# Performance work log

Hardware: AMD Instinct MI355X
Metric: run time of the kernel (lower is better)

The kernel has to match this reference:

```python
import jax, jax.numpy as jnp
import numpy as np

MUL = 32          # multiplicity of 0e and 1o channels
NRAD = 8          # radial basis size
NPATH = 7         # TP instructions

# Orthonormal symmetric-traceless basis for the real l=2 irrep -> Cartesian map
_B = np.zeros((5, 3, 3))
_s2 = 1.0 / np.sqrt(2.0)
_B[0, 0, 1] = _B[0, 1, 0] = _s2                      # xy
_B[1, 1, 2] = _B[1, 2, 1] = _s2                      # yz
_B[2] = np.diag([-1.0, -1.0, 2.0]) / np.sqrt(6.0)    # 2z^2-x^2-y^2
_B[3, 0, 2] = _B[3, 2, 0] = _s2                      # xz
_B[4] = np.diag([1.0, -1.0, 0.0]) / np.sqrt(2.0)     # x^2-y^2
# w3j(1,2,1)[i,M,k], Frobenius-normalized to 1 (e3nn convention)
C121 = jnp.asarray(np.transpose(_B, (1, 0, 2)) / np.sqrt(5.0), jnp.float32)
INV_SQRT3 = float(1.0 / np.sqrt(3.0))   # w3j(1,1,0) / w3j(0,1,1) / w3j(1,0,1)
A0 = float(1.0 / np.sqrt(64.0))         # path weight, l=0 outs: sqrt(1/fan_in), fan_in=2*32
A1 = float(np.sqrt(3.0 / 96.0))         # path weight, l=1 out: sqrt((2l+1)/fan_in), fan_in=3*32


def setup_inputs() -> dict:
    key = jax.random.key(0)
    ks = jax.random.split(key, 9)
    N, E = 4096, 32768
    x = jax.random.normal(ks[0], (N, 4 * MUL), jnp.float32)
    edge_attr = jax.random.normal(ks[1], (E, 9), jnp.float32)
    edge_length = jax.random.uniform(ks[2], (E,), jnp.float32) * 5.0
    edge_src = jax.random.randint(ks[3], (E,), 0, N)
    edge_dst = jax.random.randint(ks[4], (E,), 0, N)
    W_fc1 = jax.random.normal(ks[5], (NRAD, 64), jnp.float32)
    W_fc2 = jax.random.normal(ks[6], (64, NPATH * MUL * MUL), jnp.float32)
    W_sc_s = jax.random.normal(ks[7], (MUL, MUL), jnp.float32)
    W_sc_v = jax.random.normal(ks[8], (MUL, MUL), jnp.float32)
    return dict(x=x, edge_attr=edge_attr, edge_length=edge_length,
                edge_src=edge_src, edge_dst=edge_dst,
                W_fc1=W_fc1, W_fc2=W_fc2, W_sc_s=W_sc_s, W_sc_v=W_sc_v)


def reference(x, edge_attr, edge_length, edge_src, edge_dst, W_fc1, W_fc2, W_sc_s, W_sc_v):
    N = x.shape[0]
    # radial Gaussian basis: centers linspace(0,5,8), sigma = spacing
    centers = jnp.linspace(0.0, 5.0, NRAD)
    sigma = 5.0 / (NRAD - 1)
    d = edge_length[:, None] - centers[None, :]
    radial = jnp.exp(-d * d / (2.0 * sigma * sigma))
    # radial MLP -> per-edge TP weights (e3nn FullyConnectedNet: W/sqrt(fan_in), silu)
    h = jax.nn.silu(radial @ (W_fc1 / jnp.sqrt(jnp.float32(NRAD))))
    w = h @ (W_fc2 / jnp.sqrt(jnp.float32(64)))          # [E, 7168]
    W = w.reshape(-1, NPATH, MUL, MUL)                    # [E,7,u,w]
    # split node features: 32x0e scalars + 32x1o vectors
    s = x[:, :MUL]
    v = x[:, MUL:].reshape(N, MUL, 3)
    sj = s[edge_src]                                      # [E,u]
    vj = v[edge_src]                                      # [E,u,3]
    y0 = edge_attr[:, 0]
    y1 = edge_attr[:, 1:4]
    y2 = edge_attr[:, 4:9]
    # tensor-product paths
    t00 = sj * y0[:, None]                                            # 0e x 0e
    t11 = jnp.einsum('eui,ei->eu', vj, y1) * INV_SQRT3                # 1o x 1o -> 0e
    out_s = (jnp.einsum('eu,euw->ew', t00, W[:, 0]) +
             jnp.einsum('eu,euw->ew', t11, W[:, 1])) * A0             # scalars
    out_g = (jnp.einsum('eu,euw->ew', t00, W[:, 2]) +
             jnp.einsum('eu,euw->ew', t11, W[:, 3])) * A0             # gates
    t01 = sj[:, :, None] * y1[:, None, :] * INV_SQRT3                 # 0e x 1o -> 1o
    t10 = vj * (y0[:, None, None] * INV_SQRT3)                        # 1o x 0e -> 1o
    t12 = jnp.einsum('eui,imk,em->euk', vj, C121, y2)                 # 1o x 2e -> 1o
    out_v = (jnp.einsum('euk,euw->ewk', t01, W[:, 4]) +
             jnp.einsum('euk,euw->ewk', t10, W[:, 5]) +
             jnp.einsum('euk,euw->ewk', t12, W[:, 6])) * A1           # [E,w,3]
    m_ij = jnp.concatenate([out_s, out_g, out_v.reshape(-1, 3 * MUL)], axis=1)  # [E,160]
    # scatter-mean over destination nodes
    sums = jax.ops.segment_sum(m_ij, edge_dst, num_segments=N)
    cnt = jax.ops.segment_sum(jnp.ones((m_ij.shape[0],), m_ij.dtype), edge_dst, num_segments=N)
    m_i = sums / jnp.clip(cnt, 1.0)[:, None]
    # gate: silu on scalars, sigmoid gates multiply the 1o block per-channel
    gs = jax.nn.silu(m_i[:, :MUL])
    gate = jax.nn.sigmoid(m_i[:, MUL:2 * MUL])
    gv = m_i[:, 2 * MUL:].reshape(N, MUL, 3) * gate[:, :, None]
    # residual self-connection (e3nn o3.Linear: per-irrep, / sqrt(mul_in))
    inv_sqrt_mul = 1.0 / jnp.sqrt(jnp.float32(MUL))
    h_s = gs + (s @ W_sc_s) * inv_sqrt_mul
    h_v = gv + jnp.einsum('nui,uw->nwi', v, W_sc_v) * inv_sqrt_mul
    # o3.Norm: per-irrep L2 norm over the (2l+1) components
    norm_s = jnp.sqrt(h_s * h_s + 1e-12)
    norm_v = jnp.sqrt(jnp.sum(h_v * h_v, axis=-1) + 1e-12)
    return jnp.concatenate([norm_s, norm_v], axis=1)       # [N, 64]
```

## Files before the change

### kernel.cpp

```cpp
#include <hip/hip_runtime.h>

#define NIVL  256
#define KINV  51.2f
#define KSTEP 0.01953125f
#define TPW   7168
#define BCAP  256
#define DCAP  64
#define NROW  11
#define TSTR  40

typedef __attribute__((ext_vector_type(8))) __bf16 bf16x8;
typedef __attribute__((ext_vector_type(4))) float f32x4;
union FragU { uint4 u; bf16x8 v; };

__device__ __forceinline__ float sigmoidf_(float v) { return 1.f / (1.f + expf(-v)); }
__device__ __forceinline__ unsigned bf16r_(float x) { return (__float_as_uint(x) + 0x8000u) >> 16; }
__device__ __forceinline__ unsigned pk_(float lo, float hi) { return (bf16r_(hi) << 16) | bf16r_(lo); }

__device__ __forceinline__ f32x4 mfma_(bf16x8 a, bf16x8 b, f32x4 c) {
    return __builtin_amdgcn_mfma_f32_16x16x32_bf16(a, b, c, 0, 0, 0);
}

__global__ __launch_bounds__(256)
void prep_kernel(const float* __restrict__ W1, const float* __restrict__ W2,
                 const float* __restrict__ elen, const int* __restrict__ edst,
                 float* __restrict__ T, int* __restrict__ cntL, int* __restrict__ cntD,
                 int* __restrict__ sortedL, int* __restrict__ sortedD, int E)
{
    const int tid = threadIdx.x;
    if (blockIdx.x < 231) {
        __shared__ float hk_s[8][64];
        const int bx = blockIdx.x % 7;
        const int k0 = (blockIdx.x / 7) * 8;
        const int pw = bx * 1024 + tid * 4;
#pragma unroll
        for (int q = 0; q < 2; ++q) {
            int idx = tid + q * 256;
            int kk = idx >> 6, c = idx & 63;
            float L = (float)(k0 + kk) * KSTEP;
            float d = 0.f;
#pragma unroll
            for (int r = 0; r < 8; ++r) {
                float dd = L - (float)r * (5.f / 7.f);
                d += expf(-dd * dd * 0.98f) * W1[r * 64 + c];
            }
            d *= 0.3535533906f;
            hk_s[kk][c] = d * sigmoidf_(d) * 0.125f;
        }
        __syncthreads();
        float4 acc[8];
#pragma unroll
        for (int q = 0; q < 8; ++q) acc[q] = make_float4(0.f, 0.f, 0.f, 0.f);
        for (int c = 0; c < 64; ++c) {
            float4 w4 = *(const float4*)(W2 + (size_t)c * TPW + pw);
#pragma unroll
            for (int q = 0; q < 8; ++q) {
                float hv = hk_s[q][c];
                acc[q].x = fmaf(hv, w4.x, acc[q].x);
                acc[q].y = fmaf(hv, w4.y, acc[q].y);
                acc[q].z = fmaf(hv, w4.z, acc[q].z);
                acc[q].w = fmaf(hv, w4.w, acc[q].w);
            }
        }
#pragma unroll
        for (int q = 0; q < 8; ++q) {
            int k = k0 + q;
            if (k < 257)
                *(float4*)(T + (size_t)k * TPW + pw) = acc[q];
        }
    } else {
        int e = (blockIdx.x - 231) * 256 + tid;
        if (e < E) {
            float t = elen[e] * KINV;
            int j = (int)t; j = j > 255 ? 255 : j;
            int pos = atomicAdd(&cntL[j], 1);
            if (pos < BCAP) sortedL[j * BCAP + pos] = e;
            int d = edst[e];
            int pd = atomicAdd(&cntD[d], 1);
            if (pd < DCAP) sortedD[d * DCAP + pd] = e;
        }
    }
}

__global__ __launch_bounds__(256, 2)
void fold_kernel(const float* __restrict__ x, const float* __restrict__ ea,
                 const float* __restrict__ elen, const int* __restrict__ esrc,
                 const int* __restrict__ cntL, const int* __restrict__ sortedL,
                 const float* __restrict__ T, float* __restrict__ msg)
{
    const int j = blockIdx.x >> 1, half = blockIdx.x & 1;
    __shared__ uint4 BF[7 * 2 * 2 * 64];
    __shared__ __align__(16) unsigned short TB[2 * NROW * 16 * TSTR];
    __shared__ float EC[32][20];
    const int tid = threadIdx.x;

    const float* Trow  = T + (size_t)j * TPW;
    const float* Trow2 = Trow + TPW;
    for (int i = tid; i < 896; i += 256) {
        int pl = i >> 7, rem = i & 127;
        int whs = rem >> 6, lane_s = rem & 63;
        int u0 = (lane_s >> 4) * 8, w = whs * 16 + (lane_s & 15);
        int basei = pl * 1024 + w;
        unsigned ta[4], dd[4];
#pragma unroll
        for (int q = 0; q < 4; ++q) {
            float a0 = Trow[basei + (u0 + 2 * q) * 32];
            float a1 = Trow[basei + (u0 + 2 * q + 1) * 32];
            float b0 = Trow2[basei + (u0 + 2 * q) * 32];
            float b1 = Trow2[basei + (u0 + 2 * q + 1) * 32];
            ta[q] = pk_(a0, a1);
            dd[q] = pk_(b0 - a0, b1 - a1);
        }
        BF[(pl * 4 + whs) * 64 + lane_s]     = make_uint4(ta[0], ta[1], ta[2], ta[3]);
        BF[(pl * 4 + 2 + whs) * 64 + lane_s] = make_uint4(dd[0], dd[1], dd[2], dd[3]);
    }

    const int cnt = min(cntL[j], BCAP);
    const int nchunk = (cnt + 31) >> 5;
    const int wv = tid >> 6, lane = tid & 63;
    const int sg = wv >> 1, wh = wv & 1;
    const int col = lane & 15, quad = lane >> 4;
    const int te = tid & 31, sub = tid >> 5;
    const float I3 = 0.5773502692f, I5 = 0.4472135955f, S2 = 0.7071067812f;
    const float I6 = 0.4082482905f, T6 = 0.8164965809f;
    const float A0 = 0.125f, A1 = 0.1767766953f;

    for (int ci = half; ci < nchunk; ci += 2) {
        const int base = ci << 5;
        const int cntE = min(32, cnt - base);
        __syncthreads();
        if (tid < 32 && tid < cntE) {
            int e = sortedL[j * BCAP + base + tid];
            float L = elen[e];
            float t = L * KINV;
            int jj = (int)t; jj = jj > 255 ? 255 : jj;
            EC[tid][0] = t - (float)jj;
            EC[tid][1] = __int_as_float(esrc[e]);
            EC[tid][2] = __int_as_float(e);
            const float* y = ea + (size_t)e * 9;
            float y0 = y[0];
            EC[tid][3] = y0;
            EC[tid][4] = y0 * I3;
            EC[tid][5] = y[1] * I3;
            EC[tid][6] = y[2] * I3;
            EC[tid][7] = y[3] * I3;
            float a = y[4], b = y[5], c = y[6], d2 = y[7], ee = y[8];
            EC[tid][8]  = (-c * I6 + ee * S2) * I5;
            EC[tid][9]  = a * S2 * I5;
            EC[tid][10] = d2 * S2 * I5;
            EC[tid][11] = a * S2 * I5;
            EC[tid][12] = (-c * I6 - ee * S2) * I5;
            EC[tid][13] = b * S2 * I5;
            EC[tid][14] = d2 * S2 * I5;
            EC[tid][15] = b * S2 * I5;
            EC[tid][16] = c * T6 * I5;
        }
        __syncthreads();

        {
            const int u0 = sub * 4;
            const int esg = te >> 4, e16 = te & 15;
            float rv[NROW][4];
            if (te < cntE) {
                int src = __float_as_int(EC[te][1]);
                float y0 = EC[te][3], y0i = EC[te][4];
                float y1i0 = EC[te][5], y1i1 = EC[te][6], y1i2 = EC[te][7];
                float M0 = EC[te][8],  M1 = EC[te][9],  M2 = EC[te][10];
                float M3 = EC[te][11], M4 = EC[te][12], M5 = EC[te][13];
                float M6 = EC[te][14], M7 = EC[te][15], M8 = EC[te][16];
                const float* xp = x + (size_t)src * 128;
                float s4[4], vv[12];
                *(float4*)s4 = *(const float4*)(xp + u0);
                *(float4*)(vv)     = *(const float4*)(xp + 32 + 3 * u0);
                *(float4*)(vv + 4) = *(const float4*)(xp + 32 + 3 * u0 + 4);
                *(float4*)(vv + 8) = *(const float4*)(xp + 32 + 3 * u0 + 8);
#pragma unroll
                for (int up = 0; up < 4; ++up) {
                    float s = s4[up];
                    float v0 = vv[3 * up], v1 = vv[3 * up + 1], v2 = vv[3 * up + 2];
                    rv[0][up] = s * y0;
                    rv[1][up] = v0 * y1i0 + v1 * y1i1 + v2 * y1i2;
                    rv[2][up] = s * y1i0;
                    rv[3][up] = s * y1i1;
                    rv[4][up] = s * y1i2;
                    rv[5][up] = v0 * y0i;
                    rv[6][up] = v1 * y0i;
                    rv[7][up] = v2 * y0i;
                    rv[8][up]  = v0 * M0 + v1 * M3 + v2 * M6;
                    rv[9][up]  = v0 * M1 + v1 * M4 + v2 * M7;
                    rv[10][up] = v0 * M2 + v1 * M5 + v2 * M8;
                }
            } else {
#pragma unroll
                for (int r = 0; r < NROW; ++r)
#pragma unroll
                    for (int up = 0; up < 4; ++up) rv[r][up] = 0.f;
            }
#pragma unroll
            for (int r = 0; r < NROW; ++r) {
                unsigned lo = pk_(rv[r][0], rv[r][1]);
                unsigned hi = pk_(rv[r][2], rv[r][3]);
                *(uint2*)&TB[((esg * NROW + r) * 16 + e16) * TSTR + u0] = make_uint2(lo, hi);
            }
        }
        __syncthreads();

        f32x4 cS0 = {0,0,0,0}, cS1 = {0,0,0,0}, cG0 = {0,0,0,0}, cG1 = {0,0,0,0};
        f32x4 cV[3][2];
#pragma unroll
        for (int k = 0; k < 3; ++k) { cV[k][0] = (f32x4){0,0,0,0}; cV[k][1] = (f32x4){0,0,0,0}; }

        #define LOADA(r) ({ FragU fa_; fa_.u = *(const uint4*)&TB[((sg * NROW + (r)) * 16 + col) * TSTR + quad * 8]; fa_.v; })
        #define LOADB(p, tad) ({ FragU fb_; fb_.u = BF[((p) * 4 + (tad) * 2 + wh) * 64 + lane]; fb_.v; })

        bf16x8 a0 = LOADA(0), a1 = LOADA(1);
        cS0 = mfma_(a0, LOADB(0, 0), cS0); cS0 = mfma_(a1, LOADB(1, 0), cS0);
        cS1 = mfma_(a0, LOADB(0, 1), cS1); cS1 = mfma_(a1, LOADB(1, 1), cS1);
        cG0 = mfma_(a0, LOADB(2, 0), cG0); cG0 = mfma_(a1, LOADB(3, 0), cG0);
        cG1 = mfma_(a0, LOADB(2, 1), cG1); cG1 = mfma_(a1, LOADB(3, 1), cG1);
#pragma unroll
        for (int k = 0; k < 3; ++k) {
            bf16x8 ak;
            ak = LOADA(2 + k);
            cV[k][0] = mfma_(ak, LOADB(4, 0), cV[k][0]);
            cV[k][1] = mfma_(ak, LOADB(4, 1), cV[k][1]);
            ak = LOADA(5 + k);
            cV[k][0] = mfma_(ak, LOADB(5, 0), cV[k][0]);
            cV[k][1] = mfma_(ak, LOADB(5, 1), cV[k][1]);
            ak = LOADA(8 + k);
            cV[k][0] = mfma_(ak, LOADB(6, 0), cV[k][0]);
            cV[k][1] = mfma_(ak, LOADB(6, 1), cV[k][1]);
        }

        const int w = wh * 16 + col;
#pragma unroll
        for (int reg = 0; reg < 4; ++reg) {
            int e = sg * 16 + quad * 4 + reg;
            if (e < cntE) {
                float f = EC[e][0];
                int eid = __float_as_int(EC[e][2]);
                float* mp = msg + (size_t)eid * 160;
                mp[w]            = (cS0[reg] + f * cS1[reg]) * A0;
                mp[32 + w]       = (cG0[reg] + f * cG1[reg]) * A0;
                mp[64 + 3 * w]     = (cV[0][0][reg] + f * cV[0][1][reg]) * A1;
                mp[64 + 3 * w + 1] = (cV[1][0][reg] + f * cV[1][1][reg]) * A1;
                mp[64 + 3 * w + 2] = (cV[2][0][reg] + f * cV[2][1][reg]) * A1;
            }
        }
        #undef LOADA
        #undef LOADB
    }
}

__global__ __launch_bounds__(256)
void node_kernel(const float* __restrict__ x, const float* __restrict__ Wss,
                 const float* __restrict__ Wsv, const float* __restrict__ msg,
                 const int* __restrict__ sortedD, const int* __restrict__ cntD,
                 float* __restrict__ out, int N)
{
    __shared__ float ms[8][160];
    const int tid = threadIdx.x;
    const int n0 = blockIdx.x * 8;
    const float IM = 0.1767766953f;

#pragma unroll
    for (int it = 0; it < 5; ++it) {
        int task = tid + it * 256;
        int nl = task / 160;
        int c = task - nl * 160;
        int n = n0 + nl;
        if (n < N) {
            int cd = cntD[n];
            int cc = cd < DCAP ? cd : DCAP;
            float s = 0.f;
            for (int i = 0; i < cc; ++i)
                s += msg[(size_t)sortedD[n * DCAP + i] * 160 + c];
            ms[nl][c] = s / fmaxf((float)cd, 1.f);
        }
    }
    __syncthreads();

#pragma unroll
    for (int it = 0; it < 2; ++it) {
        int task = tid + it * 256;
        int nl = task >> 6, col = task & 63;
        int n = n0 + nl;
        if (n >= N) continue;
        const float* m  = ms[nl];
        const float* xp = x + (size_t)n * 128;
        if (col < 32) {
            int w = col;
            float mval = m[w];
            float gs = mval * sigmoidf_(mval);
            float dot = 0.f;
#pragma unroll 4
            for (int u = 0; u < 32; ++u) dot += xp[u] * Wss[u * 32 + w];
            float hs = gs + dot * IM;
            out[(size_t)n * 64 + w] = sqrtf(hs * hs + 1e-12f);
        } else {
            int w = col - 32;
            float gate = sigmoidf_(m[32 + w]);
            float g0 = m[64 + 3 * w + 0] * gate;
            float g1 = m[64 + 3 * w + 1] * gate;
            float g2 = m[64 + 3 * w + 2] * gate;
            float d0 = 0.f, d1 = 0.f, d2 = 0.f;
#pragma unroll 4
            for (int u = 0; u < 32; ++u) {
                float wv = Wsv[u * 32 + w];
                d0 += xp[32 + 3 * u + 0] * wv;
                d1 += xp[32 + 3 * u + 1] * wv;
                d2 += xp[32 + 3 * u + 2] * wv;
            }
            float h0 = g0 + d0 * IM, h1 = g1 + d1 * IM, h2 = g2 + d2 * IM;
            out[(size_t)n * 64 + 32 + w] = sqrtf(h0 * h0 + h1 * h1 + h2 * h2 + 1e-12f);
        }
    }
}

extern "C" void kernel_launch(void* const* d_in, const int* in_sizes, int n_in,
                              void* d_out, int out_size, void* d_ws, size_t ws_size,
                              hipStream_t stream)
{
    const float* x    = (const float*)d_in[0];
    const float* ea   = (const float*)d_in[1];
    const float* elen = (const float*)d_in[2];
    const int*   esrc = (const int*)d_in[3];
    const int*   edst = (const int*)d_in[4];
    const float* W1   = (const float*)d_in[5];
    const float* W2   = (const float*)d_in[6];
    const float* Wss  = (const float*)d_in[7];
    const float* Wsv  = (const float*)d_in[8];
    float* out = (float*)d_out;

    const int N = in_sizes[0] / 128;
    const int E = in_sizes[2];

    float* T      = (float*)d_ws;
    float* msg    = T + (size_t)257 * TPW;
    int*   cntL   = (int*)(msg + (size_t)E * 160);
    int*   cntD   = cntL + 256;
    int*   sortedL= cntD + N;
    int*   sortedD= sortedL + 256 * BCAP;

    hipMemsetAsync(cntL, 0, (size_t)(256 + N) * sizeof(int), stream);

    prep_kernel<<<231 + (E + 255) / 256, 256, 0, stream>>>(W1, W2, elen, edst, T, cntL, cntD, sortedL, sortedD, E);
    fold_kernel<<<NIVL * 2, 256, 0, stream>>>(x, ea, elen, esrc, cntL, sortedL, T, msg);
    node_kernel<<<(N + 7) / 8, 256, 0, stream>>>(x, Wss, Wsv, msg, sortedD, cntD, out, N);
}
```

Before: 158.8 us.

## Replace capped bucket arrays with counting-sort CSR and dst-ordered message layout

Edge bucketing moves from fixed-capacity bins (BCAP/DCAP, which silently dropped overflow) to a counting sort: the prep kernel counts, a new scan kernel builds prefix offsets, and a scatter kernel places edges. Messages are now written at destination-sorted positions, so the node kernel reads contiguous rows instead of gathering through sortedD. This adds two small kernel launches and a second round of atomics in exchange for coalesced reads in the node reduction, and it also removes the overflow truncation.

```diff
diff --git a/kernel.cpp b/kernel.cpp
--- a/kernel.cpp
+++ b/kernel.cpp
@@ -4,8 +4,6 @@
 #define KINV  51.2f
 #define KSTEP 0.01953125f
 #define TPW   7168
-#define BCAP  256
-#define DCAP  64
 #define NROW  11
 #define TSTR  40
 
@@ -24,8 +22,7 @@
 __global__ __launch_bounds__(256)
 void prep_kernel(const float* __restrict__ W1, const float* __restrict__ W2,
                  const float* __restrict__ elen, const int* __restrict__ edst,
-                 float* __restrict__ T, int* __restrict__ cntL, int* __restrict__ cntD,
-                 int* __restrict__ sortedL, int* __restrict__ sortedD, int E)
+                 float* __restrict__ T, int* __restrict__ cntL, int* __restrict__ cntD, int E)
 {
     const int tid = threadIdx.x;
     if (blockIdx.x < 231) {
@@ -73,20 +70,78 @@
         if (e < E) {
             float t = elen[e] * KINV;
             int j = (int)t; j = j > 255 ? 255 : j;
-            int pos = atomicAdd(&cntL[j], 1);
-            if (pos < BCAP) sortedL[j * BCAP + pos] = e;
-            int d = edst[e];
-            int pd = atomicAdd(&cntD[d], 1);
-            if (pd < DCAP) sortedD[d * DCAP + pd] = e;
-        }
-    }
+            atomicAdd(&cntL[j], 1);
+            atomicAdd(&cntD[edst[e]], 1);
+        }
+    }
+}
+
+__global__ __launch_bounds__(1024)
+void scan2_kernel(const int* __restrict__ cntL, const int* __restrict__ cntD,
+                  int* __restrict__ offL, int* __restrict__ curL,
+                  int* __restrict__ offD, int* __restrict__ curD)
+{
+    __shared__ int sb[1024];
+    int t = threadIdx.x;
+    if (blockIdx.x == 0) {
+        int v = (t < 256) ? cntL[t] : 0;
+        sb[t] = v;
+        __syncthreads();
+        for (int d = 1; d < 256; d <<= 1) {
+            int w = (t >= d && t < 256) ? sb[t - d] : 0;
+            __syncthreads();
+            if (t < 256) sb[t] += w;
+            __syncthreads();
+        }
+        if (t < 256) {
+            offL[t + 1] = sb[t];
+            curL[t] = sb[t] - v;
+            if (t == 0) offL[0] = 0;
+        }
+    } else {
+        int base = t * 4;
+        int v0 = cntD[base], v1 = cntD[base + 1], v2 = cntD[base + 2], v3 = cntD[base + 3];
+        int l0 = v0, l1 = l0 + v1, l2 = l1 + v2, l3 = l2 + v3;
+        sb[t] = l3;
+        __syncthreads();
+        for (int d = 1; d < 1024; d <<= 1) {
+            int w = (t >= d) ? sb[t - d] : 0;
+            __syncthreads();
+            sb[t] += w;
+            __syncthreads();
+        }
+        int gex = sb[t] - l3;
+        offD[base + 1] = gex + l0;
+        offD[base + 2] = gex + l1;
+        offD[base + 3] = gex + l2;
+        offD[base + 4] = gex + l3;
+        curD[base]     = gex;
+        curD[base + 1] = gex + l0;
+        curD[base + 2] = gex + l1;
+        curD[base + 3] = gex + l2;
+        if (t == 0) offD[0] = 0;
+    }
+}
+
+__global__ void scatter_kernel(const float* __restrict__ elen, const int* __restrict__ edst,
+                               int* __restrict__ curL, int* __restrict__ curD,
+                               int* __restrict__ sortedL, int* __restrict__ posDof, int E)
+{
+    int e = blockIdx.x * 256 + threadIdx.x;
+    if (e >= E) return;
+    float t = elen[e] * KINV;
+    int j = (int)t; j = j > 255 ? 255 : j;
+    int posL = atomicAdd(&curL[j], 1);
+    sortedL[posL] = e;
+    posDof[e] = atomicAdd(&curD[edst[e]], 1);
 }
 
 __global__ __launch_bounds__(256, 2)
 void fold_kernel(const float* __restrict__ x, const float* __restrict__ ea,
                  const float* __restrict__ elen, const int* __restrict__ esrc,
-                 const int* __restrict__ cntL, const int* __restrict__ sortedL,
-                 const float* __restrict__ T, float* __restrict__ msg)
+                 const int* __restrict__ offL, const int* __restrict__ sortedL,
+                 const int* __restrict__ posDof, const float* __restrict__ T,
+                 float* __restrict__ msg)
 {
     const int j = blockIdx.x >> 1, half = blockIdx.x & 1;
     __shared__ uint4 BF[7 * 2 * 2 * 64];
@@ -115,7 +170,8 @@
         BF[(pl * 4 + 2 + whs) * 64 + lane_s] = make_uint4(dd[0], dd[1], dd[2], dd[3]);
     }
 
-    const int cnt = min(cntL[j], BCAP);
+    const int lo = offL[j], hi = offL[j + 1];
+    const int cnt = hi - lo;
     const int nchunk = (cnt + 31) >> 5;
     const int wv = tid >> 6, lane = tid & 63;
     const int sg = wv >> 1, wh = wv & 1;
@@ -126,17 +182,17 @@
     const float A0 = 0.125f, A1 = 0.1767766953f;
 
     for (int ci = half; ci < nchunk; ci += 2) {
-        const int base = ci << 5;
-        const int cntE = min(32, cnt - base);
+        const int base = lo + (ci << 5);
+        const int cntE = min(32, hi - base);
         __syncthreads();
         if (tid < 32 && tid < cntE) {
-            int e = sortedL[j * BCAP + base + tid];
+            int e = sortedL[base + tid];
             float L = elen[e];
             float t = L * KINV;
             int jj = (int)t; jj = jj > 255 ? 255 : jj;
             EC[tid][0] = t - (float)jj;
             EC[tid][1] = __int_as_float(esrc[e]);
-            EC[tid][2] = __int_as_float(e);
+            EC[tid][2] = __int_as_float(posDof[e]);
             const float* y = ea + (size_t)e * 9;
             float y0 = y[0];
             EC[tid][3] = y0;
@@ -198,9 +254,9 @@
             }
 #pragma unroll
             for (int r = 0; r < NROW; ++r) {
-                unsigned lo = pk_(rv[r][0], rv[r][1]);
-                unsigned hi = pk_(rv[r][2], rv[r][3]);
-                *(uint2*)&TB[((esg * NROW + r) * 16 + e16) * TSTR + u0] = make_uint2(lo, hi);
+                unsigned lo2 = pk_(rv[r][0], rv[r][1]);
+                unsigned hi2 = pk_(rv[r][2], rv[r][3]);
+                *(uint2*)&TB[((esg * NROW + r) * 16 + e16) * TSTR + u0] = make_uint2(lo2, hi2);
             }
         }
         __syncthreads();
@@ -238,8 +294,8 @@
             int e = sg * 16 + quad * 4 + reg;
             if (e < cntE) {
                 float f = EC[e][0];
-                int eid = __float_as_int(EC[e][2]);
-                float* mp = msg + (size_t)eid * 160;
+                int pD = __float_as_int(EC[e][2]);
+                float* mp = msg + (size_t)pD * 160;
                 mp[w]            = (cS0[reg] + f * cS1[reg]) * A0;
                 mp[32 + w]       = (cG0[reg] + f * cG1[reg]) * A0;
                 mp[64 + 3 * w]     = (cV[0][0][reg] + f * cV[0][1][reg]) * A1;
@@ -255,8 +311,7 @@
 __global__ __launch_bounds__(256)
 void node_kernel(const float* __restrict__ x, const float* __restrict__ Wss,
                  const float* __restrict__ Wsv, const float* __restrict__ msg,
-                 const int* __restrict__ sortedD, const int* __restrict__ cntD,
-                 float* __restrict__ out, int N)
+                 const int* __restrict__ offD, float* __restrict__ out, int N)
 {
     __shared__ float ms[8][160];
     const int tid = threadIdx.x;
@@ -270,12 +325,11 @@
         int c = task - nl * 160;
         int n = n0 + nl;
         if (n < N) {
-            int cd = cntD[n];
-            int cc = cd < DCAP ? cd : DCAP;
+            int lo = offD[n], hi = offD[n + 1];
             float s = 0.f;
-            for (int i = 0; i < cc; ++i)
-                s += msg[(size_t)sortedD[n * DCAP + i] * 160 + c];
-            ms[nl][c] = s / fmaxf((float)cd, 1.f);
+            for (int r = lo; r < hi; ++r)
+                s += msg[(size_t)r * 160 + c];
+            ms[nl][c] = s / fmaxf((float)(hi - lo), 1.f);
         }
     }
     __syncthreads();
@@ -339,12 +393,18 @@
     float* msg    = T + (size_t)257 * TPW;
     int*   cntL   = (int*)(msg + (size_t)E * 160);
     int*   cntD   = cntL + 256;
-    int*   sortedL= cntD + N;
-    int*   sortedD= sortedL + 256 * BCAP;
+    int*   offL   = cntD + N;
+    int*   curL   = offL + 257;
+    int*   offD   = curL + 256;
+    int*   curD   = offD + N + 1;
+    int*   sortedL= curD + N;
+    int*   posDof = sortedL + E;
 
     hipMemsetAsync(cntL, 0, (size_t)(256 + N) * sizeof(int), stream);
 
-    prep_kernel<<<231 + (E + 255) / 256, 256, 0, stream>>>(W1, W2, elen, edst, T, cntL, cntD, sortedL, sortedD, E);
-    fold_kernel<<<NIVL * 2, 256, 0, stream>>>(x, ea, elen, esrc, cntL, sortedL, T, msg);
-    node_kernel<<<(N + 7) / 8, 256, 0, stream>>>(x, Wss, Wsv, msg, sortedD, cntD, out, N);
-}
+    prep_kernel<<<231 + (E + 255) / 256, 256, 0, stream>>>(W1, W2, elen, edst, T, cntL, cntD, E);
+    scan2_kernel<<<2, 1024, 0, stream>>>(cntL, cntD, offL, curL, offD, curD);
+    scatter_kernel<<<(E + 255) / 256, 256, 0, stream>>>(elen, edst, curL, curD, sortedL, posDof, E);
+    fold_kernel<<<NIVL * 2, 256, 0, stream>>>(x, ea, elen, esrc, offL, sortedL, posDof, T, msg);
+    node_kernel<<<(N + 7) / 8, 256, 0, stream>>>(x, Wss, Wsv, msg, offD, out, N);
+}
```

Result: slower. 169.2 us (+6.6%).

## Fuse memset, prep, fold and node kernels into one cooperative persistent kernel

Applied to the files above, without the earlier changes.

Replaces the memset and three separate kernel launches with a single cooperative kernel of 512 blocks. The blocks loop over work units for each phase and separate the phases with grid-wide syncs. Shared memory is one raw buffer reused by every phase. This is meant to remove per-launch overhead and inter-kernel gaps. In exchange it adds grid-sync costs, requires all blocks to be co-resident, and limits occupancy to the fold phase's resource needs.

```diff
diff --git a/kernel.cpp b/kernel.cpp
--- a/kernel.cpp
+++ b/kernel.cpp
@@ -1,6 +1,8 @@
 #include <hip/hip_runtime.h>
-
-#define NIVL  256
+#include <hip/hip_cooperative_groups.h>
+
+namespace cg = cooperative_groups;
+
 #define KINV  51.2f
 #define KSTEP 0.01953125f
 #define TPW   7168
@@ -21,298 +23,314 @@
     return __builtin_amdgcn_mfma_f32_16x16x32_bf16(a, b, c, 0, 0, 0);
 }
 
-__global__ __launch_bounds__(256)
-void prep_kernel(const float* __restrict__ W1, const float* __restrict__ W2,
-                 const float* __restrict__ elen, const int* __restrict__ edst,
-                 float* __restrict__ T, int* __restrict__ cntL, int* __restrict__ cntD,
-                 int* __restrict__ sortedL, int* __restrict__ sortedD, int E)
+__global__ __launch_bounds__(256, 2)
+void fused_kernel(const float* __restrict__ x, const float* __restrict__ ea,
+                  const float* __restrict__ elen, const int* __restrict__ esrc,
+                  const int* __restrict__ edst, const float* __restrict__ W1,
+                  const float* __restrict__ W2, const float* __restrict__ Wss,
+                  const float* __restrict__ Wsv, float* __restrict__ T,
+                  float* __restrict__ msg, int* __restrict__ cntL,
+                  int* __restrict__ cntD, int* __restrict__ sortedL,
+                  int* __restrict__ sortedD, float* __restrict__ out,
+                  int E, int N)
 {
-    const int tid = threadIdx.x;
-    if (blockIdx.x < 231) {
-        __shared__ float hk_s[8][64];
-        const int bx = blockIdx.x % 7;
-        const int k0 = (blockIdx.x / 7) * 8;
-        const int pw = bx * 1024 + tid * 4;
-#pragma unroll
-        for (int q = 0; q < 2; ++q) {
-            int idx = tid + q * 256;
-            int kk = idx >> 6, c = idx & 63;
-            float L = (float)(k0 + kk) * KSTEP;
-            float d = 0.f;
-#pragma unroll
-            for (int r = 0; r < 8; ++r) {
-                float dd = L - (float)r * (5.f / 7.f);
-                d += expf(-dd * dd * 0.98f) * W1[r * 64 + c];
-            }
-            d *= 0.3535533906f;
-            hk_s[kk][c] = d * sigmoidf_(d) * 0.125f;
-        }
-        __syncthreads();
-        float4 acc[8];
-#pragma unroll
-        for (int q = 0; q < 8; ++q) acc[q] = make_float4(0.f, 0.f, 0.f, 0.f);
-        for (int c = 0; c < 64; ++c) {
-            float4 w4 = *(const float4*)(W2 + (size_t)c * TPW + pw);
-#pragma unroll
-            for (int q = 0; q < 8; ++q) {
-                float hv = hk_s[q][c];
-                acc[q].x = fmaf(hv, w4.x, acc[q].x);
-                acc[q].y = fmaf(hv, w4.y, acc[q].y);
-                acc[q].z = fmaf(hv, w4.z, acc[q].z);
-                acc[q].w = fmaf(hv, w4.w, acc[q].w);
-            }
-        }
-#pragma unroll
-        for (int q = 0; q < 8; ++q) {
-            int k = k0 + q;
-            if (k < 257)
-                *(float4*)(T + (size_t)k * TPW + pw) = acc[q];
-        }
-    } else {
-        int e = (blockIdx.x - 231) * 256 + tid;
-        if (e < E) {
-            float t = elen[e] * KINV;
-            int j = (int)t; j = j > 255 ? 255 : j;
-            int pos = atomicAdd(&cntL[j], 1);
-            if (pos < BCAP) sortedL[j * BCAP + pos] = e;
-            int d = edst[e];
-            int pd = atomicAdd(&cntD[d], 1);
-            if (pd < DCAP) sortedD[d * DCAP + pd] = e;
-        }
-    }
-}
-
-__global__ __launch_bounds__(256, 2)
-void fold_kernel(const float* __restrict__ x, const float* __restrict__ ea,
-                 const float* __restrict__ elen, const int* __restrict__ esrc,
-                 const int* __restrict__ cntL, const int* __restrict__ sortedL,
-                 const float* __restrict__ T, float* __restrict__ msg)
-{
-    const int j = blockIdx.x >> 1, half = blockIdx.x & 1;
-    __shared__ uint4 BF[7 * 2 * 2 * 64];
-    __shared__ __align__(16) unsigned short TB[2 * NROW * 16 * TSTR];
-    __shared__ float EC[32][20];
-    const int tid = threadIdx.x;
-
-    const float* Trow  = T + (size_t)j * TPW;
-    const float* Trow2 = Trow + TPW;
-    for (int i = tid; i < 896; i += 256) {
-        int pl = i >> 7, rem = i & 127;
-        int whs = rem >> 6, lane_s = rem & 63;
-        int u0 = (lane_s >> 4) * 8, w = whs * 16 + (lane_s & 15);
-        int basei = pl * 1024 + w;
-        unsigned ta[4], dd[4];
-#pragma unroll
-        for (int q = 0; q < 4; ++q) {
-            float a0 = Trow[basei + (u0 + 2 * q) * 32];
-            float a1 = Trow[basei + (u0 + 2 * q + 1) * 32];
-            float b0 = Trow2[basei + (u0 + 2 * q) * 32];
-            float b1 = Trow2[basei + (u0 + 2 * q + 1) * 32];
-            ta[q] = pk_(a0, a1);
-            dd[q] = pk_(b0 - a0, b1 - a1);
-        }
-        BF[(pl * 4 + whs) * 64 + lane_s]     = make_uint4(ta[0], ta[1], ta[2], ta[3]);
-        BF[(pl * 4 + 2 + whs) * 64 + lane_s] = make_uint4(dd[0], dd[1], dd[2], dd[3]);
-    }
-
-    const int cnt = min(cntL[j], BCAP);
-    const int nchunk = (cnt + 31) >> 5;
-    const int wv = tid >> 6, lane = tid & 63;
-    const int sg = wv >> 1, wh = wv & 1;
-    const int col = lane & 15, quad = lane >> 4;
-    const int te = tid & 31, sub = tid >> 5;
+    cg::grid_group grid = cg::this_grid();
+    __shared__ __align__(16) unsigned char SMEM[59392];
+    const int tid = threadIdx.x, bid = blockIdx.x;
+    const int nb = gridDim.x;
     const float I3 = 0.5773502692f, I5 = 0.4472135955f, S2 = 0.7071067812f;
     const float I6 = 0.4082482905f, T6 = 0.8164965809f;
     const float A0 = 0.125f, A1 = 0.1767766953f;
-
-    for (int ci = half; ci < nchunk; ci += 2) {
-        const int base = ci << 5;
-        const int cntE = min(32, cnt - base);
-        __syncthreads();
-        if (tid < 32 && tid < cntE) {
-            int e = sortedL[j * BCAP + base + tid];
-            float L = elen[e];
-            float t = L * KINV;
-            int jj = (int)t; jj = jj > 255 ? 255 : jj;
-            EC[tid][0] = t - (float)jj;
-            EC[tid][1] = __int_as_float(esrc[e]);
-            EC[tid][2] = __int_as_float(e);
-            const float* y = ea + (size_t)e * 9;
-            float y0 = y[0];
-            EC[tid][3] = y0;
-            EC[tid][4] = y0 * I3;
-            EC[tid][5] = y[1] * I3;
-            EC[tid][6] = y[2] * I3;
-            EC[tid][7] = y[3] * I3;
-            float a = y[4], b = y[5], c = y[6], d2 = y[7], ee = y[8];
-            EC[tid][8]  = (-c * I6 + ee * S2) * I5;
-            EC[tid][9]  = a * S2 * I5;
-            EC[tid][10] = d2 * S2 * I5;
-            EC[tid][11] = a * S2 * I5;
-            EC[tid][12] = (-c * I6 - ee * S2) * I5;
-            EC[tid][13] = b * S2 * I5;
-            EC[tid][14] = d2 * S2 * I5;
-            EC[tid][15] = b * S2 * I5;
-            EC[tid][16] = c * T6 * I5;
-        }
-        __syncthreads();
-
-        {
-            const int u0 = sub * 4;
-            const int esg = te >> 4, e16 = te & 15;
-            float rv[NROW][4];
-            if (te < cntE) {
-                int src = __float_as_int(EC[te][1]);
-                float y0 = EC[te][3], y0i = EC[te][4];
-                float y1i0 = EC[te][5], y1i1 = EC[te][6], y1i2 = EC[te][7];
-                float M0 = EC[te][8],  M1 = EC[te][9],  M2 = EC[te][10];
-                float M3 = EC[te][11], M4 = EC[te][12], M5 = EC[te][13];
-                float M6 = EC[te][14], M7 = EC[te][15], M8 = EC[te][16];
-                const float* xp = x + (size_t)src * 128;
-                float s4[4], vv[12];
-                *(float4*)s4 = *(const float4*)(xp + u0);
-                *(float4*)(vv)     = *(const float4*)(xp + 32 + 3 * u0);
-                *(float4*)(vv + 4) = *(const float4*)(xp + 32 + 3 * u0 + 4);
-                *(float4*)(vv + 8) = *(const float4*)(xp + 32 + 3 * u0 + 8);
-#pragma unroll
-                for (int up = 0; up < 4; ++up) {
-                    float s = s4[up];
-                    float v0 = vv[3 * up], v1 = vv[3 * up + 1], v2 = vv[3 * up + 2];
-                    rv[0][up] = s * y0;
-                    rv[1][up] = v0 * y1i0 + v1 * y1i1 + v2 * y1i2;
-                    rv[2][up] = s * y1i0;
-                    rv[3][up] = s * y1i1;
-                    rv[4][up] = s * y1i2;
-                    rv[5][up] = v0 * y0i;
-                    rv[6][up] = v1 * y0i;
-                    rv[7][up] = v2 * y0i;
-                    rv[8][up]  = v0 * M0 + v1 * M3 + v2 * M6;
-                    rv[9][up]  = v0 * M1 + v1 * M4 + v2 * M7;
-                    rv[10][up] = v0 * M2 + v1 * M5 + v2 * M8;
+    const float IM = 0.1767766953f;
+
+    for (int gt = bid * 256 + tid; gt < 256 + N; gt += nb * 256) cntL[gt] = 0;
+    __threadfence();
+    grid.sync();
+
+    {
+        const int nscat = (E + 255) >> 8;
+        for (int unit = bid; unit < 231 + nscat; unit += nb) {
+            if (unit < 231) {
+                float (*hk_s)[64] = (float (*)[64])SMEM;
+                const int bx = unit % 7;
+                const int k0 = (unit / 7) * 8;
+                const int pw = bx * 1024 + tid * 4;
+                __syncthreads();
+#pragma unroll
+                for (int q = 0; q < 2; ++q) {
+                    int idx = tid + q * 256;
+                    int kk = idx >> 6, c = idx & 63;
+                    float L = (float)(k0 + kk) * KSTEP;
+                    float d = 0.f;
+#pragma unroll
+                    for (int r = 0; r < 8; ++r) {
+                        float dd = L - (float)r * (5.f / 7.f);
+                        d += expf(-dd * dd * 0.98f) * W1[r * 64 + c];
+                    }
+                    d *= 0.3535533906f;
+                    hk_s[kk][c] = d * sigmoidf_(d) * 0.125f;
+                }
+                __syncthreads();
+                float4 acc[8];
+#pragma unroll
+                for (int q = 0; q < 8; ++q) acc[q] = make_float4(0.f, 0.f, 0.f, 0.f);
+                for (int c = 0; c < 64; ++c) {
+                    float4 w4 = *(const float4*)(W2 + (size_t)c * TPW + pw);
+#pragma unroll
+                    for (int q = 0; q < 8; ++q) {
+                        float hv = hk_s[q][c];
+                        acc[q].x = fmaf(hv, w4.x, acc[q].x);
+                        acc[q].y = fmaf(hv, w4.y, acc[q].y);
+                        acc[q].z = fmaf(hv, w4.z, acc[q].z);
+                        acc[q].w = fmaf(hv, w4.w, acc[q].w);
+                    }
+                }
+#pragma unroll
+                for (int q = 0; q < 8; ++q) {
+                    int k = k0 + q;
+                    if (k < 257)
+                        *(float4*)(T + (size_t)k * TPW + pw) = acc[q];
                 }
             } else {
-#pragma unroll
-                for (int r = 0; r < NROW; ++r)
-#pragma unroll
-                    for (int up = 0; up < 4; ++up) rv[r][up] = 0.f;
-            }
-#pragma unroll
-            for (int r = 0; r < NROW; ++r) {
-                unsigned lo = pk_(rv[r][0], rv[r][1]);
-                unsigned hi = pk_(rv[r][2], rv[r][3]);
-                *(uint2*)&TB[((esg * NROW + r) * 16 + e16) * TSTR + u0] = make_uint2(lo, hi);
-            }
-        }
-        __syncthreads();
-
-        f32x4 cS0 = {0,0,0,0}, cS1 = {0,0,0,0}, cG0 = {0,0,0,0}, cG1 = {0,0,0,0};
-        f32x4 cV[3][2];
-#pragma unroll
-        for (int k = 0; k < 3; ++k) { cV[k][0] = (f32x4){0,0,0,0}; cV[k][1] = (f32x4){0,0,0,0}; }
-
-        #define LOADA(r) ({ FragU fa_; fa_.u = *(const uint4*)&TB[((sg * NROW + (r)) * 16 + col) * TSTR + quad * 8]; fa_.v; })
-        #define LOADB(p, tad) ({ FragU fb_; fb_.u = BF[((p) * 4 + (tad) * 2 + wh) * 64 + lane]; fb_.v; })
-
-        bf16x8 a0 = LOADA(0), a1 = LOADA(1);
-        cS0 = mfma_(a0, LOADB(0, 0), cS0); cS0 = mfma_(a1, LOADB(1, 0), cS0);
-        cS1 = mfma_(a0, LOADB(0, 1), cS1); cS1 = mfma_(a1, LOADB(1, 1), cS1);
-        cG0 = mfma_(a0, LOADB(2, 0), cG0); cG0 = mfma_(a1, LOADB(3, 0), cG0);
-        cG1 = mfma_(a0, LOADB(2, 1), cG1); cG1 = mfma_(a1, LOADB(3, 1), cG1);
-#pragma unroll
-        for (int k = 0; k < 3; ++k) {
-            bf16x8 ak;
-            ak = LOADA(2 + k);
-            cV[k][0] = mfma_(ak, LOADB(4, 0), cV[k][0]);
-            cV[k][1] = mfma_(ak, LOADB(4, 1), cV[k][1]);
-            ak = LOADA(5 + k);
-            cV[k][0] = mfma_(ak, LOADB(5, 0), cV[k][0]);
-            cV[k][1] = mfma_(ak, LOADB(5, 1), cV[k][1]);
-            ak = LOADA(8 + k);
-            cV[k][0] = mfma_(ak, LOADB(6, 0), cV[k][0]);
-            cV[k][1] = mfma_(ak, LOADB(6, 1), cV[k][1]);
-        }
-
-        const int w = wh * 16 + col;
-#pragma unroll
-        for (int reg = 0; reg < 4; ++reg) {
-            int e = sg * 16 + quad * 4 + reg;
-            if (e < cntE) {
-                float f = EC[e][0];
-                int eid = __float_as_int(EC[e][2]);
-                float* mp = msg + (size_t)eid * 160;
-                mp[w]            = (cS0[reg] + f * cS1[reg]) * A0;
-                mp[32 + w]       = (cG0[reg] + f * cG1[reg]) * A0;
-                mp[64 + 3 * w]     = (cV[0][0][reg] + f * cV[0][1][reg]) * A1;
-                mp[64 + 3 * w + 1] = (cV[1][0][reg] + f * cV[1][1][reg]) * A1;
-                mp[64 + 3 * w + 2] = (cV[2][0][reg] + f * cV[2][1][reg]) * A1;
-            }
-        }
-        #undef LOADA
-        #undef LOADB
-    }
-}
-
-__global__ __launch_bounds__(256)
-void node_kernel(const float* __restrict__ x, const float* __restrict__ Wss,
-                 const float* __restrict__ Wsv, const float* __restrict__ msg,
-                 const int* __restrict__ sortedD, const int* __restrict__ cntD,
-                 float* __restrict__ out, int N)
-{
-    __shared__ float ms[8][160];
-    const int tid = threadIdx.x;
-    const int n0 = blockIdx.x * 8;
-    const float IM = 0.1767766953f;
-
-#pragma unroll
-    for (int it = 0; it < 5; ++it) {
-        int task = tid + it * 256;
-        int nl = task / 160;
-        int c = task - nl * 160;
-        int n = n0 + nl;
-        if (n < N) {
-            int cd = cntD[n];
-            int cc = cd < DCAP ? cd : DCAP;
-            float s = 0.f;
-            for (int i = 0; i < cc; ++i)
-                s += msg[(size_t)sortedD[n * DCAP + i] * 160 + c];
-            ms[nl][c] = s / fmaxf((float)cd, 1.f);
+                int e = (unit - 231) * 256 + tid;
+                if (e < E) {
+                    float t = elen[e] * KINV;
+                    int j = (int)t; j = j > 255 ? 255 : j;
+                    int pos = atomicAdd(&cntL[j], 1);
+                    if (pos < BCAP) sortedL[j * BCAP + pos] = e;
+                    int dn = edst[e];
+                    int pd = atomicAdd(&cntD[dn], 1);
+                    if (pd < DCAP) sortedD[dn * DCAP + pd] = e;
+                }
+            }
         }
     }
-    __syncthreads();
-
-#pragma unroll
-    for (int it = 0; it < 2; ++it) {
-        int task = tid + it * 256;
-        int nl = task >> 6, col = task & 63;
-        int n = n0 + nl;
-        if (n >= N) continue;
-        const float* m  = ms[nl];
-        const float* xp = x + (size_t)n * 128;
-        if (col < 32) {
-            int w = col;
-            float mval = m[w];
-            float gs = mval * sigmoidf_(mval);
-            float dot = 0.f;
+    __threadfence();
+    grid.sync();
+
+    {
+        uint4* BF = (uint4*)SMEM;
+        unsigned short* TB = (unsigned short*)(SMEM + 28672);
+        float (*EC)[20] = (float (*)[20])(SMEM + 28672 + 28160);
+        const int wv = tid >> 6, lane = tid & 63;
+        const int sg = wv >> 1, wh = wv & 1;
+        const int col = lane & 15, quad = lane >> 4;
+        const int te = tid & 31, sub = tid >> 5;
+
+        for (int unit = bid; unit < 512; unit += nb) {
+            const int j = unit >> 1, half = unit & 1;
+            __syncthreads();
+            const float* Trow  = T + (size_t)j * TPW;
+            const float* Trow2 = Trow + TPW;
+            for (int i = tid; i < 896; i += 256) {
+                int pl = i >> 7, rem = i & 127;
+                int whs = rem >> 6, lane_s = rem & 63;
+                int u0 = (lane_s >> 4) * 8, w = whs * 16 + (lane_s & 15);
+                int basei = pl * 1024 + w;
+                unsigned ta[4], dd[4];
+#pragma unroll
+                for (int q = 0; q < 4; ++q) {
+                    float a0 = Trow[basei + (u0 + 2 * q) * 32];
+                    float a1 = Trow[basei + (u0 + 2 * q + 1) * 32];
+                    float b0 = Trow2[basei + (u0 + 2 * q) * 32];
+                    float b1 = Trow2[basei + (u0 + 2 * q + 1) * 32];
+                    ta[q] = pk_(a0, a1);
+                    dd[q] = pk_(b0 - a0, b1 - a1);
+                }
+                BF[(pl * 4 + whs) * 64 + lane_s]     = make_uint4(ta[0], ta[1], ta[2], ta[3]);
+                BF[(pl * 4 + 2 + whs) * 64 + lane_s] = make_uint4(dd[0], dd[1], dd[2], dd[3]);
+            }
+
+            const int cnt = min(cntL[j], BCAP);
+            const int nchunk = (cnt + 31) >> 5;
+
+            for (int ci = half; ci < nchunk; ci += 2) {
+                const int base = ci << 5;
+                const int cntE = min(32, cnt - base);
+                __syncthreads();
+                if (tid < 32 && tid < cntE) {
+                    int e = sortedL[j * BCAP + base + tid];
+                    float L = elen[e];
+                    float t = L * KINV;
+                    int jj = (int)t; jj = jj > 255 ? 255 : jj;
+                    EC[tid][0] = t - (float)jj;
+                    EC[tid][1] = __int_as_float(esrc[e]);
+                    EC[tid][2] = __int_as_float(e);
+                    const float* y = ea + (size_t)e * 9;
+                    float y0 = y[0];
+                    EC[tid][3] = y0;
+                    EC[tid][4] = y0 * I3;
+                    EC[tid][5] = y[1] * I3;
+                    EC[tid][6] = y[2] * I3;
+                    EC[tid][7] = y[3] * I3;
+                    float a = y[4], b = y[5], c = y[6], d2 = y[7], ee = y[8];
+                    EC[tid][8]  = (-c * I6 + ee * S2) * I5;
+                    EC[tid][9]  = a * S2 * I5;
+                    EC[tid][10] = d2 * S2 * I5;
+                    EC[tid][11] = a * S2 * I5;
+                    EC[tid][12] = (-c * I6 - ee * S2) * I5;
+                    EC[tid][13] = b * S2 * I5;
+                    EC[tid][14] = d2 * S2 * I5;
+                    EC[tid][15] = b * S2 * I5;
+                    EC[tid][16] = c * T6 * I5;
+                }
+                __syncthreads();
+
+                {
+                    const int u0 = sub * 4;
+                    const int esg = te >> 4, e16 = te & 15;
+                    float rv[NROW][4];
+                    if (te < cntE) {
+                        int src = __float_as_int(EC[te][1]);
+                        float y0 = EC[te][3], y0i = EC[te][4];
+                        float y1i0 = EC[te][5], y1i1 = EC[te][6], y1i2 = EC[te][7];
+                        float M0 = EC[te][8],  M1 = EC[te][9],  M2 = EC[te][10];
+                        float M3 = EC[te][11], M4 = EC[te][12], M5 = EC[te][13];
+                        float M6 = EC[te][14], M7 = EC[te][15], M8 = EC[te][16];
+                        const float* xp = x + (size_t)src * 128;
+                        float s4[4], vvv[12];
+                        *(float4*)s4 = *(const float4*)(xp + u0);
+                        *(float4*)(vvv)     = *(const float4*)(xp + 32 + 3 * u0);
+                        *(float4*)(vvv + 4) = *(const float4*)(xp + 32 + 3 * u0 + 4);
+                        *(float4*)(vvv + 8) = *(const float4*)(xp + 32 + 3 * u0 + 8);
+#pragma unroll
+                        for (int up = 0; up < 4; ++up) {
+                            float s = s4[up];
+                            float v0 = vvv[3 * up], v1 = vvv[3 * up + 1], v2 = vvv[3 * up + 2];
+                            rv[0][up] = s * y0;
+                            rv[1][up] = v0 * y1i0 + v1 * y1i1 + v2 * y1i2;
+                            rv[2][up] = s * y1i0;
+                            rv[3][up] = s * y1i1;
+                            rv[4][up] = s * y1i2;
+                            rv[5][up] = v0 * y0i;
+                            rv[6][up] = v1 * y0i;
+                            rv[7][up] = v2 * y0i;
+                            rv[8][up]  = v0 * M0 + v1 * M3 + v2 * M6;
+                            rv[9][up]  = v0 * M1 + v1 * M4 + v2 * M7;
+                            rv[10][up] = v0 * M2 + v1 * M5 + v2 * M8;
+                        }
+                    } else {
+#pragma unroll
+                        for (int r = 0; r < NROW; ++r)
+#pragma unroll
+                            for (int up = 0; up < 4; ++up) rv[r][up] = 0.f;
+                    }
+#pragma unroll
+                    for (int r = 0; r < NROW; ++r) {
+                        unsigned lo2 = pk_(rv[r][0], rv[r][1]);
+                        unsigned hi2 = pk_(rv[r][2], rv[r][3]);
+                        *(uint2*)&TB[((esg * NROW + r) * 16 + e16) * TSTR + u0] = make_uint2(lo2, hi2);
+                    }
+                }
+                __syncthreads();
+
+                f32x4 cS0 = {0,0,0,0}, cS1 = {0,0,0,0}, cG0 = {0,0,0,0}, cG1 = {0,0,0,0};
+                f32x4 cV[3][2];
+#pragma unroll
+                for (int k = 0; k < 3; ++k) { cV[k][0] = (f32x4){0,0,0,0}; cV[k][1] = (f32x4){0,0,0,0}; }
+
+                #define LOADA(r) ({ FragU fa_; fa_.u = *(const uint4*)&TB[((sg * NROW + (r)) * 16 + col) * TSTR + quad * 8]; fa_.v; })
+                #define LOADB(p, tad) ({ FragU fb_; fb_.u = BF[((p) * 4 + (tad) * 2 + wh) * 64 + lane]; fb_.v; })
+
+                bf16x8 a0 = LOADA(0), a1 = LOADA(1);
+                cS0 = mfma_(a0, LOADB(0, 0), cS0); cS0 = mfma_(a1, LOADB(1, 0), cS0);
+                cS1 = mfma_(a0, LOADB(0, 1), cS1); cS1 = mfma_(a1, LOADB(1, 1), cS1);
+                cG0 = mfma_(a0, LOADB(2, 0), cG0); cG0 = mfma_(a1, LOADB(3, 0), cG0);
+                cG1 = mfma_(a0, LOADB(2, 1), cG1); cG1 = mfma_(a1, LOADB(3, 1), cG1);
+#pragma unroll
+                for (int k = 0; k < 3; ++k) {
+                    bf16x8 ak;
+                    ak = LOADA(2 + k);
+                    cV[k][0] = mfma_(ak, LOADB(4, 0), cV[k][0]);
+                    cV[k][1] = mfma_(ak, LOADB(4, 1), cV[k][1]);
+                    ak = LOADA(5 + k);
+                    cV[k][0] = mfma_(ak, LOADB(5, 0), cV[k][0]);
+                    cV[k][1] = mfma_(ak, LOADB(5, 1), cV[k][1]);
+                    ak = LOADA(8 + k);
+                    cV[k][0] = mfma_(ak, LOADB(6, 0), cV[k][0]);
+                    cV[k][1] = mfma_(ak, LOADB(6, 1), cV[k][1]);
+                }
+
+                const int w = wh * 16 + col;
+#pragma unroll
+                for (int reg = 0; reg < 4; ++reg) {
+                    int e = sg * 16 + quad * 4 + reg;
+                    if (e < cntE) {
+                        float f = EC[e][0];
+                        int eid = __float_as_int(EC[e][2]);
+                        float* mp = msg + (size_t)eid * 160;
+                        mp[w]            = (cS0[reg] + f * cS1[reg]) * A0;
+                        mp[32 + w]       = (cG0[reg] + f * cG1[reg]) * A0;
+                        mp[64 + 3 * w]     = (cV[0][0][reg] + f * cV[0][1][reg]) * A1;
+                        mp[64 + 3 * w + 1] = (cV[1][0][reg] + f * cV[1][1][reg]) * A1;
+                        mp[64 + 3 * w + 2] = (cV[2][0][reg] + f * cV[2][1][reg]) * A1;
+                    }
+                }
+                #undef LOADA
+                #undef LOADB
+            }
+        }
+    }
+    __threadfence();
+    grid.sync();
+
+    {
+        float (*ms)[160] = (float (*)[160])SMEM;
+        const int nunits = (N + 7) >> 3;
+        for (int unit = bid; unit < nunits; unit += nb) {
+            const int n0 = unit * 8;
+            __syncthreads();
+#pragma unroll
+            for (int it = 0; it < 5; ++it) {
+                int task = tid + it * 256;
+                int nl = task / 160;
+                int c = task - nl * 160;
+                int n = n0 + nl;
+                if (n < N) {
+                    int cd = cntD[n];
+                    int cc = cd < DCAP ? cd : DCAP;
+                    float s = 0.f;
+                    for (int i = 0; i < cc; ++i)
+                        s += msg[(size_t)sortedD[n * DCAP + i] * 160 + c];
+                    ms[nl][c] = s / fmaxf((float)cd, 1.f);
+                }
+            }
+            __syncthreads();
+#pragma unroll
+            for (int it = 0; it < 2; ++it) {
+                int task = tid + it * 256;
+                int nl = task >> 6, c2 = task & 63;
+                int n = n0 + nl;
+                if (n >= N) continue;
+                const float* m  = ms[nl];
+                const float* xp = x + (size_t)n * 128;
+                if (c2 < 32) {
+                    int w = c2;
+                    float mval = m[w];
+                    float gs = mval * sigmoidf_(mval);
+                    float dot = 0.f;
 #pragma unroll 4
-            for (int u = 0; u < 32; ++u) dot += xp[u] * Wss[u * 32 + w];
-            float hs = gs + dot * IM;
-            out[(size_t)n * 64 + w] = sqrtf(hs * hs + 1e-12f);
-        } else {
-            int w = col - 32;
-            float gate = sigmoidf_(m[32 + w]);
-            float g0 = m[64 + 3 * w + 0] * gate;
-            float g1 = m[64 + 3 * w + 1] * gate;
-            float g2 = m[64 + 3 * w + 2] * gate;
-            float d0 = 0.f, d1 = 0.f, d2 = 0.f;
+                    for (int u = 0; u < 32; ++u) dot += xp[u] * Wss[u * 32 + w];
+                    float hs = gs + dot * IM;
+                    out[(size_t)n * 64 + w] = sqrtf(hs * hs + 1e-12f);
+                } else {
+                    int w = c2 - 32;
+                    float gate = sigmoidf_(m[32 + w]);
+                    float g0 = m[64 + 3 * w + 0] * gate;
+                    float g1 = m[64 + 3 * w + 1] * gate;
+                    float g2 = m[64 + 3 * w + 2] * gate;
+                    float d0 = 0.f, d1 = 0.f, d2 = 0.f;
 #pragma unroll 4
-            for (int u = 0; u < 32; ++u) {
-                float wv = Wsv[u * 32 + w];
-                d0 += xp[32 + 3 * u + 0] * wv;
-                d1 += xp[32 + 3 * u + 1] * wv;
-                d2 += xp[32 + 3 * u + 2] * wv;
-            }
-            float h0 = g0 + d0 * IM, h1 = g1 + d1 * IM, h2 = g2 + d2 * IM;
-            out[(size_t)n * 64 + 32 + w] = sqrtf(h0 * h0 + h1 * h1 + h2 * h2 + 1e-12f);
+                    for (int u = 0; u < 32; ++u) {
+                        float wv = Wsv[u * 32 + w];
+                        d0 += xp[32 + 3 * u + 0] * wv;
+                        d1 += xp[32 + 3 * u + 1] * wv;
+                        d2 += xp[32 + 3 * u + 2] * wv;
+                    }
+                    float h0 = g0 + d0 * IM, h1 = g1 + d1 * IM, h2 = g2 + d2 * IM;
+                    out[(size_t)n * 64 + 32 + w] = sqrtf(h0 * h0 + h1 * h1 + h2 * h2 + 1e-12f);
+                }
+            }
         }
     }
 }
@@ -332,8 +350,8 @@
     const float* Wsv  = (const float*)d_in[8];
     float* out = (float*)d_out;
 
-    const int N = in_sizes[0] / 128;
-    const int E = in_sizes[2];
+    int N = in_sizes[0] / 128;
+    int E = in_sizes[2];
 
     float* T      = (float*)d_ws;
     float* msg    = T + (size_t)257 * TPW;
@@ -342,9 +360,8 @@
     int*   sortedL= cntD + N;
     int*   sortedD= sortedL + 256 * BCAP;
 
-    hipMemsetAsync(cntL, 0, (size_t)(256 + N) * sizeof(int), stream);
-
-    prep_kernel<<<231 + (E + 255) / 256, 256, 0, stream>>>(W1, W2, elen, edst, T, cntL, cntD, sortedL, sortedD, E);
-    fold_kernel<<<NIVL * 2, 256, 0, stream>>>(x, ea, elen, esrc, cntL, sortedL, T, msg);
-    node_kernel<<<(N + 7) / 8, 256, 0, stream>>>(x, Wss, Wsv, msg, sortedD, cntD, out, N);
+    void* args[] = { &x, &ea, &elen, &esrc, &edst, &W1, &W2, &Wss, &Wsv,
+                     &T, &msg, &cntL, &cntD, &sortedL, &sortedD, &out, &E, &N };
+    hipLaunchCooperativeKernel((const void*)fused_kernel, dim3(512), dim3(256),
+                               args, 0, stream);
 }
```

After: 437.7 us. 2.76x slower.
